# Optimization experiments

Hardware: AMD Instinct MI355X
Metric: run time of the kernel (lower is better)

Reference implementation:

```python
import jax, jax.numpy as jnp
import numpy as np

EPS = 1e-15
MAX_TANH_ARG = 1.0 - 1e-5  # clamp for artanh domain, standard in Poincare-ball libs


def logmap0(x):
    # Poincare ball, c=1: logmap0(x) = artanh(||x||) * x / ||x||
    norm = jnp.linalg.norm(x, axis=-1, keepdims=True)
    norm_c = jnp.clip(norm, EPS, MAX_TANH_ARG)
    scale = jnp.arctanh(norm_c) / jnp.maximum(norm, EPS)
    return scale * x


def expmap0(v):
    # Poincare ball, c=1: expmap0(v) = tanh(||v||) * v / ||v||
    norm = jnp.linalg.norm(v, axis=-1, keepdims=True)
    scale = jnp.tanh(norm) / jnp.maximum(norm, EPS)
    return scale * v


def setup_inputs() -> dict:
    key = jax.random.key(0)
    k1, k2, k3, k4 = jax.random.split(key, 4)
    N, E, D_IN, D_OUT = 50000, 600000, 128, 128
    # points loosely inside/near the ball; logmap0 clamps the norm anyway
    x = jax.random.uniform(k1, (N, D_IN), dtype=jnp.float32)
    edge_index = jax.random.randint(k2, (2, E), 0, N, dtype=jnp.int32)
    W = jax.random.normal(k3, (D_OUT, D_IN), dtype=jnp.float32) / np.sqrt(D_IN)
    b = jax.random.normal(k4, (D_OUT,), dtype=jnp.float32) * 0.01
    return {"x": x, "edge_index": edge_index, "W": W, "b": b}


def reference(x, edge_index, W, b):
    num_nodes = x.shape[0]
    src, dst = edge_index[0], edge_index[1]

    x_tangent = logmap0(x)                       # [N, D_in]
    h = x_tangent @ W.T + b                      # [N, D_out]

    # symmetric degree count: each edge adds 1 to dst and 1 to src
    ones = jnp.ones(src.shape[0], dtype=jnp.float32)
    deg = (jax.ops.segment_sum(ones, dst, num_segments=num_nodes)
           + jax.ops.segment_sum(ones, src, num_segments=num_nodes))
    deg = jnp.maximum(deg, 1.0)
    dinv = deg ** -0.5                           # [N]

    # fused gather-scale-scatter across ALL feature dims at once
    msg = h[src] * (dinv[src] * dinv[dst])[:, None]   # [E, D_out]
    out = jax.ops.segment_sum(msg, dst, num_segments=num_nodes)  # [N, D_out]

    return expmap0(out)
```

## Files before the change

### kernel.cpp

```cpp
#include <hip/hip_runtime.h>
#include <math.h>

#define D 128
#define CAP 48
#define NS 128
#define HBT (NS * 2)
#define HLDSB 57344
#define BKB 128

typedef __attribute__((ext_vector_type(8))) short short8;
typedef __attribute__((ext_vector_type(4))) float f32x4;

__device__ inline unsigned short f2bf(float f) {
  unsigned int u = __float_as_uint(f);
  u = (u + 0x7FFFu + ((u >> 16) & 1u)) >> 16;
  return (unsigned short)u;
}
__device__ inline float bf2f(unsigned int us) {
  return __uint_as_float(us << 16);
}

__global__ __launch_bounds__(1024) void k_prep(
    const float* __restrict__ W, const int* __restrict__ src,
    const int* __restrict__ dst, unsigned short* __restrict__ Wbf,
    unsigned int* __restrict__ cursor, unsigned char* __restrict__ part8,
    unsigned char* __restrict__ rank, int N, int E, int HP, int fancy) {
  const int t = threadIdx.x;
  const int bid = blockIdx.x;

  if (bid < HBT) {
    if (!fancy) return;
    __shared__ unsigned int lh[HLDSB / 4];
    const int kind = bid >> 7;
    const int s = bid & (NS - 1);
    const int G16 = (N + 15) >> 4;
    for (int i = t; i < G16; i += 1024) ((uint4*)lh)[i] = make_uint4(0, 0, 0, 0);
    __syncthreads();
    const int e0 = (int)((long long)s * E / NS);
    const int e1 = (int)((long long)(s + 1) * E / NS);
    if (kind == 0) {
      for (int e = e0 + t; e < e1; e += 1024) {
        unsigned int n = (unsigned)dst[e];
        int sh = (n & 3) << 3;
        unsigned int old = atomicAdd(&lh[n >> 2], 1u << sh);
        rank[e] = (unsigned char)((old >> sh) & 0xFFu);
      }
    } else {
      for (int e = e0 + t; e < e1; e += 1024) {
        unsigned int n = (unsigned)src[e];
        atomicAdd(&lh[n >> 2], 1u << ((n & 3) << 3));
      }
    }
    __syncthreads();
    uint4* po = (uint4*)(part8 + (size_t)bid * HP);
    for (int i = t; i < G16; i += 1024) po[i] = ((const uint4*)lh)[i];
    return;
  }

  int g = (bid - HBT) * 1024 + t;
  if (g < N) cursor[g] = 0u;
  int i = g * 4;
  if (i < D * D) {
    float4 wv = *(const float4*)(W + i);
    int r = i >> 7, c = i & 127;
    int idx = ((c >> 3) << 10) + (r << 3) + (c & 7);
    *(ushort4*)(&Wbf[idx]) =
        make_ushort4(f2bf(wv.x), f2bf(wv.y), f2bf(wv.z), f2bf(wv.w));
  }
}

__global__ __launch_bounds__(256) void k_reduce(
    const unsigned char* __restrict__ part8, float* __restrict__ dinv,
    unsigned int* __restrict__ cntv, unsigned int* __restrict__ pre32, int N,
    int HP) {
  int n = blockIdx.x * 256 + threadIdx.x;
  if (n >= N) return;
  unsigned int run = 0, so = 0;
#pragma unroll 8
  for (int g = 0; g < NS / 2; ++g) {
    unsigned int c0 = part8[(size_t)(2 * g) * HP + n];
    unsigned int c1 = part8[(size_t)(2 * g + 1) * HP + n];
    unsigned int o0 = part8[(size_t)(NS + 2 * g) * HP + n];
    unsigned int o1 = part8[(size_t)(NS + 2 * g + 1) * HP + n];
    unsigned int w = run & 0xFFFFu;
    run += c0;
    w |= (run & 0xFFFFu) << 16;
    run += c1;
    so += o0 + o1;
    pre32[(size_t)g * N + n] = w;
  }
  cntv[n] = run;
  dinv[n] = rsqrtf(fmaxf((float)(run + so), 1.0f));
}

__global__ __launch_bounds__(256) void k_main(
    const float* __restrict__ x, const unsigned short* __restrict__ Wbf,
    const float* __restrict__ bvec, const int* __restrict__ src,
    const int* __restrict__ dst, unsigned int* __restrict__ cursor,
    int* __restrict__ ebuf, const unsigned char* __restrict__ rank,
    const unsigned int* __restrict__ pre32, unsigned short* __restrict__ h,
    int N, int E, int fancy) {
  const int t = threadIdx.x;
  const int bid = blockIdx.x;

  if (bid < BKB) {
    if (fancy) {
      const int s = bid;
      const int e0 = (int)((long long)s * E / NS);
      const int e1 = (int)((long long)(s + 1) * E / NS);
      const unsigned int* ps = pre32 + (size_t)(s >> 1) * N;
      const int sh = (s & 1) << 4;
      for (int e = e0 + t; e < e1; e += 256) {
        int d_ = dst[e];
        unsigned int slot = ((ps[d_] >> sh) & 0xFFFFu) + (unsigned int)rank[e];
        if (slot < CAP) ebuf[(size_t)d_ * CAP + slot] = src[e];
      }
    } else {
      const int e0 = (int)((long long)bid * E / BKB);
      const int e1 = (int)((long long)(bid + 1) * E / BKB);
      for (int e = e0 + t; e < e1; e += 256) {
        int d_ = dst[e], s_ = src[e];
        unsigned int p = atomicAdd(&cursor[d_], 1u) & 0xFFFFu;
        if (p < CAP) ebuf[(size_t)d_ * CAP + p] = s_;
        atomicAdd(&cursor[s_], 0x10000u);
      }
    }
    return;
  }

  const int gb = bid - BKB;
  const int w = t >> 6;
  const int l = t & 63;
  const int lc = l & 15;
  const int q = l >> 4;
  const int r0 = gb * 64;
  const int grow = r0 + w * 16 + lc;
  const bool ok = grow < N;
  const float* xp = x + (size_t)grow * D + q * 8;

  short8 a[4];
  float ss = 0.0f;
#pragma unroll
  for (int kk = 0; kk < 4; ++kk) {
    float4 u = ok ? *(const float4*)(xp + kk * 32) : make_float4(0, 0, 0, 0);
    float4 v = ok ? *(const float4*)(xp + kk * 32 + 4) : make_float4(0, 0, 0, 0);
    ss += u.x * u.x + u.y * u.y + u.z * u.z + u.w * u.w;
    ss += v.x * v.x + v.y * v.y + v.z * v.z + v.w * v.w;
    short8 af;
    af[0] = (short)f2bf(u.x); af[1] = (short)f2bf(u.y);
    af[2] = (short)f2bf(u.z); af[3] = (short)f2bf(u.w);
    af[4] = (short)f2bf(v.x); af[5] = (short)f2bf(v.y);
    af[6] = (short)f2bf(v.z); af[7] = (short)f2bf(v.w);
    a[kk] = af;
  }
  ss += __shfl_xor(ss, 16, 64);
  ss += __shfl_xor(ss, 32, 64);
  float nrm = sqrtf(ss);
  float nc = fminf(fmaxf(nrm, 1e-15f), 1.0f - 1e-5f);
  float rs = atanhf(nc) / fmaxf(nrm, 1e-15f);

  f32x4 acc[8];
#pragma unroll
  for (int nt = 0; nt < 8; ++nt) acc[nt] = (f32x4){0.f, 0.f, 0.f, 0.f};

#pragma unroll
  for (int kk = 0; kk < 4; ++kk) {
#pragma unroll
    for (int nt = 0; nt < 8; ++nt) {
      short8 bf =
          *(const short8*)(Wbf + ((kk * 4 + q) << 10) + ((nt * 16 + lc) << 3));
      acc[nt] = __builtin_amdgcn_mfma_f32_16x16x32_bf16(a[kk], bf, acc[nt], 0, 0, 0);
    }
  }

  float rsl[4];
#pragma unroll
  for (int i = 0; i < 4; ++i) rsl[i] = __shfl(rs, q * 4 + i, 64);

#pragma unroll
  for (int nt = 0; nt < 8; ++nt) {
    int j = nt * 16 + lc;
    float bj = bvec[j];
#pragma unroll
    for (int i = 0; i < 4; ++i) {
      int gr = r0 + w * 16 + q * 4 + i;
      if (gr < N) h[(size_t)gr * D + j] = f2bf(rsl[i] * acc[nt][i] + bj);
    }
  }
}

__global__ __launch_bounds__(256) void k_gather(
    const unsigned short* __restrict__ h, const int* __restrict__ ebuf,
    const unsigned int* __restrict__ cursor, const float* __restrict__ dinv,
    const unsigned int* __restrict__ cntv, float* __restrict__ out, int N,
    int fancy) {
  int gid = blockIdx.x * 256 + threadIdx.x;
  int r = gid >> 5;
  int sub = threadIdx.x & 31;
  if (r >= N) return;

  int cnt;
  float di_d;
  if (fancy) {
    cnt = (int)cntv[r];
    di_d = dinv[r];
  } else {
    unsigned int cr = cursor[r];
    cnt = (int)(cr & 0xFFFFu);
    di_d = rsqrtf(fmaxf((float)((cr & 0xFFFFu) + (cr >> 16)), 1.0f));
  }
  if (cnt > CAP) cnt = CAP;
  const int* eb = ebuf + (size_t)r * CAP;

  int c1 = cnt < 32 ? cnt : 32;
  int s_a = (sub < c1) ? eb[sub] : 0;
  float dv_a = 0.0f;
  if (sub < c1) {
    if (fancy) dv_a = dinv[s_a];
    else {
      unsigned int vs = cursor[s_a];
      dv_a = rsqrtf(fmaxf((float)((vs & 0xFFFFu) + (vs >> 16)), 1.0f));
    }
  }
  int s_b = (sub + 32 < cnt) ? eb[32 + sub] : 0;
  float dv_b = 0.0f;
  if (sub + 32 < cnt) {
    if (fancy) dv_b = dinv[s_b];
    else {
      unsigned int vs = cursor[s_b];
      dv_b = rsqrtf(fmaxf((float)((vs & 0xFFFFu) + (vs >> 16)), 1.0f));
    }
  }

  float a0 = 0.f, a1 = 0.f, a2 = 0.f, a3 = 0.f;
  for (int i = 0; i < c1; i += 8) {
    uint2 pv[8];
    float wj[8];
#pragma unroll
    for (int j = 0; j < 8; ++j) {
      int s = __shfl(s_a, i + j, 32);
      wj[j] = __shfl(dv_a, i + j, 32);
      pv[j] = *(const uint2*)(h + (size_t)s * D + sub * 4);
    }
#pragma unroll
    for (int j = 0; j < 8; ++j) {
      a0 += wj[j] * bf2f(pv[j].x & 0xFFFFu);
      a1 += wj[j] * bf2f(pv[j].x >> 16);
      a2 += wj[j] * bf2f(pv[j].y & 0xFFFFu);
      a3 += wj[j] * bf2f(pv[j].y >> 16);
    }
  }
  for (int i = 0; i < cnt - 32; i += 8) {
    uint2 pv[8];
    float wj[8];
#pragma unroll
    for (int j = 0; j < 8; ++j) {
      int s = __shfl(s_b, i + j, 32);
      wj[j] = __shfl(dv_b, i + j, 32);
      pv[j] = *(const uint2*)(h + (size_t)s * D + sub * 4);
    }
#pragma unroll
    for (int j = 0; j < 8; ++j) {
      a0 += wj[j] * bf2f(pv[j].x & 0xFFFFu);
      a1 += wj[j] * bf2f(pv[j].x >> 16);
      a2 += wj[j] * bf2f(pv[j].y & 0xFFFFu);
      a3 += wj[j] * bf2f(pv[j].y >> 16);
    }
  }

  a0 *= di_d; a1 *= di_d; a2 *= di_d; a3 *= di_d;

  float sN = a0 * a0 + a1 * a1 + a2 * a2 + a3 * a3;
#pragma unroll
  for (int off = 16; off > 0; off >>= 1) sN += __shfl_down(sN, off, 32);
  sN = __shfl(sN, 0, 32);
  float n = sqrtf(sN);
  float sc = tanhf(n) / fmaxf(n, 1e-15f);

  float4* op = (float4*)(out + (size_t)r * D);
  op[sub] = make_float4(a0 * sc, a1 * sc, a2 * sc, a3 * sc);
}

extern "C" void kernel_launch(void* const* d_in, const int* in_sizes, int n_in,
                              void* d_out, int out_size, void* d_ws, size_t ws_size,
                              hipStream_t stream) {
  const float* x = (const float*)d_in[0];
  const int* ei = (const int*)d_in[1];
  const float* W = (const float*)d_in[2];
  const float* b = (const float*)d_in[3];
  float* out = (float*)d_out;

  const int N = in_sizes[0] / D;
  const int E = in_sizes[1] / 2;
  const int* src = ei;
  const int* dst = ei + E;

  const int HP = (N + 255) & ~255;

  size_t o_ebuf = ((size_t)N * D * 2 + 63) & ~(size_t)63;
  size_t o_cur = (o_ebuf + (size_t)N * CAP * 4 + 63) & ~(size_t)63;
  size_t o_dinv = (o_cur + (size_t)N * 4 + 63) & ~(size_t)63;
  size_t o_cnt = (o_dinv + (size_t)N * 4 + 63) & ~(size_t)63;
  size_t o_wbf = (o_cnt + (size_t)N * 4 + 63) & ~(size_t)63;
  size_t o_p8 = (o_wbf + 32768 + 255) & ~(size_t)255;
  size_t o_pre = (o_p8 + (size_t)HBT * HP + 63) & ~(size_t)63;
  size_t o_rank = (o_pre + (size_t)(NS / 2) * N * 4 + 63) & ~(size_t)63;
  size_t need = o_rank + (size_t)E;

  unsigned short* h = (unsigned short*)d_ws;
  int* ebuf = (int*)((char*)d_ws + o_ebuf);
  unsigned int* cursor = (unsigned int*)((char*)d_ws + o_cur);
  float* dinv = (float*)((char*)d_ws + o_dinv);
  unsigned int* cntv = (unsigned int*)((char*)d_ws + o_cnt);
  unsigned short* Wbf = (unsigned short*)((char*)d_ws + o_wbf);
  unsigned char* part8 = (unsigned char*)((char*)d_ws + o_p8);
  unsigned int* pre32 = (unsigned int*)((char*)d_ws + o_pre);
  unsigned char* rank = (unsigned char*)((char*)d_ws + o_rank);

  const int fancy = (N <= HLDSB) && (N <= 65535) && (ws_size >= need);

  int PB = (N + 1023) / 1024;
  if (PB < 4) PB = 4;
  k_prep<<<HBT + PB, 1024, 0, stream>>>(W, src, dst, Wbf, cursor, part8, rank,
                                        N, E, HP, fancy);

  if (fancy)
    k_reduce<<<(N + 255) / 256, 256, 0, stream>>>(part8, dinv, cntv, pre32, N,
                                                  HP);

  const int NBG = (N + 63) / 64;
  k_main<<<BKB + NBG, 256, 0, stream>>>(x, Wbf, b, src, dst, cursor, ebuf, rank,
                                        pre32, h, N, E, fancy);
  k_gather<<<(int)(((long long)N * 32 + 255) / 256), 256, 0, stream>>>(
      h, ebuf, cursor, dinv, cntv, out, N, fancy);
}
```

Baseline: 141.2 us.

## Pack source degree scale into edge buffer and shrink per-slice prefix offsets

```diff
diff --git a/kernel.cpp b/kernel.cpp
--- a/kernel.cpp
+++ b/kernel.cpp
@@ -58,7 +58,7 @@
   }
 
   int g = (bid - HBT) * 1024 + t;
-  if (g < N) cursor[g] = 0u;
+  if (!fancy && g < N) cursor[g] = 0u;
   int i = g * 4;
   if (i < D * D) {
     float4 wv = *(const float4*)(W + i);
@@ -71,35 +71,28 @@
 
 __global__ __launch_bounds__(256) void k_reduce(
     const unsigned char* __restrict__ part8, float* __restrict__ dinv,
-    unsigned int* __restrict__ cntv, unsigned int* __restrict__ pre32, int N,
-    int HP) {
+    int2* __restrict__ meta, unsigned char* __restrict__ pre8, int N, int HP) {
   int n = blockIdx.x * 256 + threadIdx.x;
   if (n >= N) return;
   unsigned int run = 0, so = 0;
 #pragma unroll 8
-  for (int g = 0; g < NS / 2; ++g) {
-    unsigned int c0 = part8[(size_t)(2 * g) * HP + n];
-    unsigned int c1 = part8[(size_t)(2 * g + 1) * HP + n];
-    unsigned int o0 = part8[(size_t)(NS + 2 * g) * HP + n];
-    unsigned int o1 = part8[(size_t)(NS + 2 * g + 1) * HP + n];
-    unsigned int w = run & 0xFFFFu;
-    run += c0;
-    w |= (run & 0xFFFFu) << 16;
-    run += c1;
-    so += o0 + o1;
-    pre32[(size_t)g * N + n] = w;
-  }
-  cntv[n] = run;
-  dinv[n] = rsqrtf(fmaxf((float)(run + so), 1.0f));
+  for (int s = 0; s < NS; ++s) {
+    pre8[(size_t)s * N + n] = (unsigned char)run;
+    run += part8[(size_t)s * HP + n];
+    so += part8[(size_t)(NS + s) * HP + n];
+  }
+  float dv = rsqrtf(fmaxf((float)(run + so), 1.0f));
+  dinv[n] = dv;
+  meta[n] = make_int2((int)run, __float_as_int(dv));
 }
 
 __global__ __launch_bounds__(256) void k_main(
     const float* __restrict__ x, const unsigned short* __restrict__ Wbf,
     const float* __restrict__ bvec, const int* __restrict__ src,
     const int* __restrict__ dst, unsigned int* __restrict__ cursor,
-    int* __restrict__ ebuf, const unsigned char* __restrict__ rank,
-    const unsigned int* __restrict__ pre32, unsigned short* __restrict__ h,
-    int N, int E, int fancy) {
+    int2* __restrict__ ebuf2, const unsigned char* __restrict__ rank,
+    const unsigned char* __restrict__ pre8, const float* __restrict__ dinv,
+    unsigned short* __restrict__ h, int N, int E, int fancy) {
   const int t = threadIdx.x;
   const int bid = blockIdx.x;
 
@@ -108,12 +101,15 @@
       const int s = bid;
       const int e0 = (int)((long long)s * E / NS);
       const int e1 = (int)((long long)(s + 1) * E / NS);
-      const unsigned int* ps = pre32 + (size_t)(s >> 1) * N;
-      const int sh = (s & 1) << 4;
+      const unsigned char* ps = pre8 + (size_t)s * N;
       for (int e = e0 + t; e < e1; e += 256) {
         int d_ = dst[e];
-        unsigned int slot = ((ps[d_] >> sh) & 0xFFFFu) + (unsigned int)rank[e];
-        if (slot < CAP) ebuf[(size_t)d_ * CAP + slot] = src[e];
+        unsigned int slot = (unsigned int)ps[d_] + (unsigned int)rank[e];
+        if (slot < CAP) {
+          int s_ = src[e];
+          ebuf2[(size_t)d_ * CAP + slot] =
+              make_int2(s_, __float_as_int(dinv[s_]));
+        }
       }
     } else {
       const int e0 = (int)((long long)bid * E / BKB);
@@ -121,7 +117,7 @@
       for (int e = e0 + t; e < e1; e += 256) {
         int d_ = dst[e], s_ = src[e];
         unsigned int p = atomicAdd(&cursor[d_], 1u) & 0xFFFFu;
-        if (p < CAP) ebuf[(size_t)d_ * CAP + p] = s_;
+        if (p < CAP) ebuf2[(size_t)d_ * CAP + p] = make_int2(s_, 0);
         atomicAdd(&cursor[s_], 0x10000u);
       }
     }
@@ -190,10 +186,9 @@
 }
 
 __global__ __launch_bounds__(256) void k_gather(
-    const unsigned short* __restrict__ h, const int* __restrict__ ebuf,
-    const unsigned int* __restrict__ cursor, const float* __restrict__ dinv,
-    const unsigned int* __restrict__ cntv, float* __restrict__ out, int N,
-    int fancy) {
+    const unsigned short* __restrict__ h, const int2* __restrict__ ebuf2,
+    const unsigned int* __restrict__ cursor, const int2* __restrict__ meta,
+    float* __restrict__ out, int N, int fancy) {
   int gid = blockIdx.x * 256 + threadIdx.x;
   int r = gid >> 5;
   int sub = threadIdx.x & 31;
@@ -202,31 +197,33 @@
   int cnt;
   float di_d;
   if (fancy) {
-    cnt = (int)cntv[r];
-    di_d = dinv[r];
+    int2 mt = meta[r];
+    cnt = mt.x;
+    di_d = __int_as_float(mt.y);
   } else {
     unsigned int cr = cursor[r];
     cnt = (int)(cr & 0xFFFFu);
     di_d = rsqrtf(fmaxf((float)((cr & 0xFFFFu) + (cr >> 16)), 1.0f));
   }
   if (cnt > CAP) cnt = CAP;
-  const int* eb = ebuf + (size_t)r * CAP;
+  const int2* eb = ebuf2 + (size_t)r * CAP;
 
   int c1 = cnt < 32 ? cnt : 32;
-  int s_a = (sub < c1) ? eb[sub] : 0;
-  float dv_a = 0.0f;
-  if (sub < c1) {
-    if (fancy) dv_a = dinv[s_a];
-    else {
+  int2 ea = (sub < c1) ? eb[sub] : make_int2(0, 0);
+  int2 eb_ = (sub + 32 < cnt) ? eb[32 + sub] : make_int2(0, 0);
+  int s_a = ea.x, s_b = eb_.x;
+  float dv_a, dv_b;
+  if (fancy) {
+    dv_a = __int_as_float(ea.y);
+    dv_b = __int_as_float(eb_.y);
+  } else {
+    dv_a = 0.0f;
+    if (sub < c1) {
       unsigned int vs = cursor[s_a];
       dv_a = rsqrtf(fmaxf((float)((vs & 0xFFFFu) + (vs >> 16)), 1.0f));
     }
-  }
-  int s_b = (sub + 32 < cnt) ? eb[32 + sub] : 0;
-  float dv_b = 0.0f;
-  if (sub + 32 < cnt) {
-    if (fancy) dv_b = dinv[s_b];
-    else {
+    dv_b = 0.0f;
+    if (sub + 32 < cnt) {
       unsigned int vs = cursor[s_b];
       dv_b = rsqrtf(fmaxf((float)((vs & 0xFFFFu) + (vs >> 16)), 1.0f));
     }
@@ -298,39 +295,44 @@
   const int HP = (N + 255) & ~255;
 
   size_t o_ebuf = ((size_t)N * D * 2 + 63) & ~(size_t)63;
-  size_t o_cur = (o_ebuf + (size_t)N * CAP * 4 + 63) & ~(size_t)63;
+  size_t o_cur = (o_ebuf + (size_t)N * CAP * 8 + 63) & ~(size_t)63;
   size_t o_dinv = (o_cur + (size_t)N * 4 + 63) & ~(size_t)63;
-  size_t o_cnt = (o_dinv + (size_t)N * 4 + 63) & ~(size_t)63;
-  size_t o_wbf = (o_cnt + (size_t)N * 4 + 63) & ~(size_t)63;
+  size_t o_meta = (o_dinv + (size_t)N * 4 + 63) & ~(size_t)63;
+  size_t o_wbf = (o_meta + (size_t)N * 8 + 63) & ~(size_t)63;
   size_t o_p8 = (o_wbf + 32768 + 255) & ~(size_t)255;
   size_t o_pre = (o_p8 + (size_t)HBT * HP + 63) & ~(size_t)63;
-  size_t o_rank = (o_pre + (size_t)(NS / 2) * N * 4 + 63) & ~(size_t)63;
+  size_t o_rank = (o_pre + (size_t)NS * N + 63) & ~(size_t)63;
   size_t need = o_rank + (size_t)E;
 
   unsigned short* h = (unsigned short*)d_ws;
-  int* ebuf = (int*)((char*)d_ws + o_ebuf);
+  int2* ebuf2 = (int2*)((char*)d_ws + o_ebuf);
   unsigned int* cursor = (unsigned int*)((char*)d_ws + o_cur);
   float* dinv = (float*)((char*)d_ws + o_dinv);
-  unsigned int* cntv = (unsigned int*)((char*)d_ws + o_cnt);
+  int2* meta = (int2*)((char*)d_ws + o_meta);
   unsigned short* Wbf = (unsigned short*)((char*)d_ws + o_wbf);
   unsigned char* part8 = (unsigned char*)((char*)d_ws + o_p8);
-  unsigned int* pre32 = (unsigned int*)((char*)d_ws + o_pre);
+  unsigned char* pre8 = (unsigned char*)((char*)d_ws + o_pre);
   unsigned char* rank = (unsigned char*)((char*)d_ws + o_rank);
 
   const int fancy = (N <= HLDSB) && (N <= 65535) && (ws_size >= need);
 
-  int PB = (N + 1023) / 1024;
-  if (PB < 4) PB = 4;
+  int PB;
+  if (fancy) {
+    PB = 4;
+  } else {
+    PB = (N + 1023) / 1024;
+    if (PB < 4) PB = 4;
+  }
   k_prep<<<HBT + PB, 1024, 0, stream>>>(W, src, dst, Wbf, cursor, part8, rank,
                                         N, E, HP, fancy);
 
   if (fancy)
-    k_reduce<<<(N + 255) / 256, 256, 0, stream>>>(part8, dinv, cntv, pre32, N,
+    k_reduce<<<(N + 255) / 256, 256, 0, stream>>>(part8, dinv, meta, pre8, N,
                                                   HP);
 
   const int NBG = (N + 63) / 64;
-  k_main<<<BKB + NBG, 256, 0, stream>>>(x, Wbf, b, src, dst, cursor, ebuf, rank,
-                                        pre32, h, N, E, fancy);
+  k_main<<<BKB + NBG, 256, 0, stream>>>(x, Wbf, b, src, dst, cursor, ebuf2,
+                                        rank, pre8, dinv, h, N, E, fancy);
   k_gather<<<(int)(((long long)N * 32 + 255) / 256), 256, 0, stream>>>(
-      h, ebuf, cursor, dinv, cntv, out, N, fancy);
-}
+      h, ebuf2, cursor, meta, out, N, fancy);
+}
```

Measured after the change: 140.9 us. Within noise of the previous version (-0.2%).
